# Kernel optimization log

Hardware: AMD Instinct MI355X
Metric: run time of the kernel (lower is better)

## Reference

```python
import math
import jax, jax.numpy as jnp
import numpy as np

B, LA, LB, H = 16, 1024, 1024, 512
NEG = -10000000.0


def setup_inputs() -> dict:
    key = jax.random.key(0)
    k1, k2, k3, k4 = jax.random.split(key, 4)
    a = jax.random.normal(k1, (B, LA, H), dtype=jnp.float32)
    b = jax.random.normal(k2, (B, LB, H), dtype=jnp.float32)
    mask_a = jax.random.randint(k3, (B, LA, 1), 0, 2, dtype=jnp.int32)
    mask_b = jax.random.randint(k4, (B, LB, 1), 0, 2, dtype=jnp.int32)
    temperature = jnp.asarray(1.0 / math.sqrt(H), dtype=jnp.float32)
    return {"a": a, "b": b, "mask_a": mask_a, "mask_b": mask_b, "temperature": temperature}


def reference(a, b, mask_a, mask_b, temperature):
    # attn[b,i,j] = <a_i, b_j> * temperature  -> [B, LA, LB]
    attn = jnp.einsum("bid,bjd->bij", a, b) * temperature
    # pairwise validity mask: outer product of per-token masks
    mask = jnp.einsum("bik,bjk->bij", mask_a.astype(jnp.float32), mask_b.astype(jnp.float32)) > 0
    attn = jnp.where(mask, attn, NEG)
    attn_a = jax.nn.softmax(attn, axis=1)  # softmax over a-tokens
    attn_b = jax.nn.softmax(attn, axis=2)  # softmax over b-tokens
    feature_b = jnp.einsum("bij,bid->bjd", attn_a, a)  # [B, LB, H]
    feature_a = jnp.einsum("bij,bjd->bid", attn_b, b)  # [B, LA, H]
    return (feature_a, feature_b)
```

## Files before the change

kernel.cpp:

```cpp
#include <hip/hip_runtime.h>
#include <hip/hip_bf16.h>

#define NB_ 16
#define LA_ 1024
#define LB_ 1024
#define H_  512

typedef __attribute__((ext_vector_type(8))) short short8;
typedef __attribute__((ext_vector_type(4))) float f32x4;

using bf16 = __hip_bfloat16;

__device__ __forceinline__ float bf2f(unsigned short u) {
    union { unsigned int i; float f; } c; c.i = ((unsigned)u) << 16; return c.f;
}
__device__ __forceinline__ unsigned short f2bf(float f) {
    bf16 h = __float2bfloat16(f);
    return *(unsigned short*)&h;
}

__device__ __forceinline__ void load_lds16(const void* g, void* l) {
    __builtin_amdgcn_global_load_lds(
        (const __attribute__((address_space(1))) void*)g,
        (__attribute__((address_space(3))) void*)l, 16, 0, 0);
}

template<int DB, int MODE>
__device__ __forceinline__ void gemm_tile256(
    const unsigned short* __restrict__ gA, const unsigned short* __restrict__ gB,
    int lda, int ldb, size_t ko,
    unsigned short* lds, char* lA, char* lB,
    const int* aoff, const int* boff, f32x4 acc[8][4])
{
    const char* bA = (const char*)lds + DB * 32768;
    const char* bB = (const char*)lds + 65536 + DB * 32768;
    const int nxt = (DB ^ 1) * 32768;
    short8 av[4][2];
#pragma unroll
    for (int p = 0; p < 4; ++p) {
        const int pm = p >> 1, pn = p & 1;
        if (pn == 0) {
#pragma unroll
            for (int f = 0; f < 4; f++)
#pragma unroll
                for (int kk = 0; kk < 2; kk++)
                    av[f][kk] = *(const short8*)(bA + (aoff[pm * 4 + f] ^ (kk << 6)));
        }
        short8 bv[2][2];
#pragma unroll
        for (int f = 0; f < 2; f++)
#pragma unroll
            for (int kk = 0; kk < 2; kk++)
                bv[f][kk] = *(const short8*)(bB + (boff[pn * 2 + f] ^ (kk << 6)));
        if (MODE == 0) {
            if (p == 0) {
                load_lds16(gB + ko,                       lB + nxt);
                load_lds16(gB + ko + (size_t)64 * ldb,    lB + nxt + 8192);
            } else if (p == 1) {
                load_lds16(gB + ko + (size_t)128 * ldb,   lB + nxt + 16384);
                load_lds16(gB + ko + (size_t)192 * ldb,   lB + nxt + 24576);
            } else if (p == 2) {
                load_lds16(gA + ko,                       lA + nxt);
                load_lds16(gA + ko + (size_t)128 * lda,   lA + nxt + 16384);
            } else {
                load_lds16(gA + ko + (size_t)64 * lda,    lA + nxt + 8192);
                load_lds16(gA + ko + (size_t)192 * lda,   lA + nxt + 24576);
            }
        }
        __builtin_amdgcn_s_barrier();
        __builtin_amdgcn_s_setprio(1);
#pragma unroll
        for (int kk = 0; kk < 2; kk++)
#pragma unroll
            for (int f = 0; f < 2; f++)
#pragma unroll
                for (int m = 0; m < 4; m++)
                    acc[pm * 4 + m][pn * 2 + f] =
                        __builtin_amdgcn_mfma_f32_16x16x32_bf16(
                            av[m][kk], bv[f][kk],
                            acc[pm * 4 + m][pn * 2 + f], 0, 0, 0);
        __builtin_amdgcn_s_setprio(0);
        if (p == 1) {
            if (MODE == 0) asm volatile("s_waitcnt vmcnt(4)" ::: "memory");
            else           asm volatile("s_waitcnt vmcnt(0)" ::: "memory");
        }
        if (p == 3 && MODE == 0) asm volatile("s_waitcnt vmcnt(2)" ::: "memory");
        if (p < 3 || MODE == 0) __builtin_amdgcn_s_barrier();
    }
}

__device__ __forceinline__ void gemm_core256(
    const unsigned short* __restrict__ A, const unsigned short* __restrict__ B,
    int lda, int ldb, int K,
    unsigned short* lds, f32x4 acc[8][4])
{
    const int t = threadIdx.x;
    const int w = t >> 6, lane = t & 63;
    const int wr = w >> 2, wc = w & 3;
    const int lm = lane & 15, q = lane >> 4;

    int aoff[8], boff[4];
#pragma unroll
    for (int f = 0; f < 8; f++) {
        const int ra = wr * 128 + f * 16 + lm;
        aoff[f] = ra * 128 + ((q ^ (ra & 7)) << 4);
    }
#pragma unroll
    for (int f = 0; f < 4; f++) {
        const int rb = wc * 64 + f * 16 + lm;
        boff[f] = rb * 128 + ((q ^ (rb & 7)) << 4);
    }

    const int rstep = w * 8 + (lane >> 3);
    const int sc = (lane & 7) ^ (lane >> 3);
    const unsigned short* gA = A + (size_t)rstep * lda + sc * 8;
    const unsigned short* gB = B + (size_t)rstep * ldb + sc * 8;
    char* lA = (char*)lds + w * 1024;
    char* lB = (char*)lds + 65536 + w * 1024;
    const int NT = K >> 6;

    load_lds16(gB,                       lB);
    load_lds16(gB + (size_t)64 * ldb,    lB + 8192);
    load_lds16(gB + (size_t)128 * ldb,   lB + 16384);
    load_lds16(gB + (size_t)192 * ldb,   lB + 24576);
    load_lds16(gA,                       lA);
    load_lds16(gA + (size_t)128 * lda,   lA + 16384);
    load_lds16(gA + (size_t)64 * lda,    lA + 8192);
    load_lds16(gA + (size_t)192 * lda,   lA + 24576);
    asm volatile("s_waitcnt vmcnt(2)" ::: "memory");
    __builtin_amdgcn_s_barrier();

    int kt = 0;
    for (; kt + 2 < NT; kt += 2) {
        gemm_tile256<0, 0>(gA, gB, lda, ldb, (size_t)(kt + 1) * 64,
                           lds, lA, lB, aoff, boff, acc);
        gemm_tile256<1, 0>(gA, gB, lda, ldb, (size_t)(kt + 2) * 64,
                           lds, lA, lB, aoff, boff, acc);
    }
    gemm_tile256<0, 0>(gA, gB, lda, ldb, (size_t)(NT - 1) * 64,
                       lds, lA, lB, aoff, boff, acc);
    gemm_tile256<1, 1>(gA, gB, lda, ldb, 0, lds, lA, lB, aoff, boff, acc);
    __syncthreads();
}

__global__ __launch_bounds__(512, 2) void k_gemm_attn(
    const unsigned short* __restrict__ a_bf, const unsigned short* __restrict__ b_bf,
    const int* __restrict__ mask_a, const int* __restrict__ mask_b,
    const float* __restrict__ temp_p,
    unsigned short* __restrict__ E, unsigned short* __restrict__ ET,
    float* __restrict__ l_row, float* __restrict__ l_col)
{
    __shared__ unsigned short lds[65536];

    const int g = blockIdx.x;
    const int batch = g & 15;
    const int qq = g >> 4;
    const int i0 = (qq >> 2) * 256, j0 = (qq & 3) * 256;

    const unsigned short* A = a_bf + (size_t)batch * LA_ * H_ + (size_t)i0 * H_;
    const unsigned short* B = b_bf + (size_t)batch * LB_ * H_ + (size_t)j0 * H_;
    f32x4 acc[8][4];
#pragma unroll
    for (int x = 0; x < 8; x++)
#pragma unroll
        for (int y = 0; y < 4; y++) acc[x][y] = 0;

    gemm_core256(A, B, H_, H_, H_, lds, acc);

    const float temp = temp_p[0];
    const int t = threadIdx.x, w = t >> 6, lane = t & 63;
    const int wr = w >> 2, wc = w & 3, lm = lane & 15, q = lane >> 4;
    const int* map = mask_a + batch * LA_;
    const int* mbp = mask_b + batch * LB_;
    unsigned short* Ep  = E  + (size_t)batch * LA_ * LB_;
    unsigned short* ETp = ET + (size_t)batch * LB_ * LA_;
    float* lrp = l_row + batch * LA_;
    float* lcp = l_col + batch * LB_;

    int mb4[4];
#pragma unroll
    for (int fn = 0; fn < 4; fn++) mb4[fn] = mbp[j0 + wc * 64 + fn * 16 + lm];

#pragma unroll
    for (int fm = 0; fm < 8; fm++) {
        const int ilb = wr * 128 + fm * 16 + q * 4;
        int ma[4];
#pragma unroll
        for (int r = 0; r < 4; r++) ma[r] = map[i0 + ilb + r];
#pragma unroll
        for (int fn = 0; fn < 4; fn++) {
            const int jl = wc * 64 + fn * 16 + lm;
            ushort4 pk;
            unsigned short* pp = (unsigned short*)&pk;
#pragma unroll
            for (int r = 0; r < 4; r++) {
                const float e = (ma[r] && mb4[fn]) ? __expf(acc[fm][fn][r] * temp) : 0.0f;
                acc[fm][fn][r] = e;
                pp[r] = f2bf(e);
                const int il = ilb + r;
                lds[il * 256 + ((((jl >> 3) ^ ((il >> 1) & 15)) << 3) | (jl & 7))] = pp[r];
            }
            *(ushort4*)(ETp + (size_t)(j0 + jl) * LA_ + i0 + ilb) = pk;
        }
    }

#pragma unroll
    for (int fm = 0; fm < 8; fm++)
#pragma unroll
        for (int r = 0; r < 4; r++) {
            float s = acc[fm][0][r] + acc[fm][1][r] + acc[fm][2][r] + acc[fm][3][r];
            s += __shfl_xor(s, 1, 16); s += __shfl_xor(s, 2, 16);
            s += __shfl_xor(s, 4, 16); s += __shfl_xor(s, 8, 16);
            if (lm == 0) atomicAdd(&lrp[i0 + wr * 128 + fm * 16 + q * 4 + r], s);
        }
#pragma unroll
    for (int fn = 0; fn < 4; fn++) {
        float s = 0.0f;
#pragma unroll
        for (int fm = 0; fm < 8; fm++)
#pragma unroll
            for (int r = 0; r < 4; r++) s += acc[fm][fn][r];
        s += __shfl_xor(s, 16, 64); s += __shfl_xor(s, 32, 64);
        if (lane < 16) atomicAdd(&lcp[j0 + wc * 64 + fn * 16 + lm], s);
    }

    __syncthreads();
#pragma unroll
    for (int rep = 0; rep < 16; rep++) {
        const int il = (t >> 5) + rep * 16;
        const int c = t & 31;
        const int phys = c ^ ((il >> 1) & 15);
        short8 v = *(const short8*)(lds + il * 256 + phys * 8);
        *(short8*)(Ep + (size_t)(i0 + il) * LB_ + j0 + c * 8) = v;
    }
}

__global__ __launch_bounds__(512, 2) void k_gemm_feat(
    const unsigned short* __restrict__ E, const unsigned short* __restrict__ ET,
    const unsigned short* __restrict__ aT, const unsigned short* __restrict__ bT,
    const int* __restrict__ mask_a, const int* __restrict__ mask_b,
    const int* __restrict__ nA, const int* __restrict__ nB,
    const float* __restrict__ l_row, const float* __restrict__ l_col,
    const float* __restrict__ mean_a, const float* __restrict__ mean_b,
    float* __restrict__ out)
{
    __shared__ unsigned short lds[65536];

    const int g = blockIdx.x;
    const int zc = g & 31;
    const int qq = g >> 5;
    const int n0 = (qq & 1) * 256, m0 = (qq >> 1) * 256;

    const int batch = zc & 15;
    const bool isA = zc < 16;
    const unsigned short* Amat = (isA ? E : ET) + (size_t)batch * 1024 * 1024;
    const unsigned short* Bm   = (isA ? bT : aT) + (size_t)batch * H_ * 1024;
    const int* mp   = (isA ? mask_a : mask_b) + batch * 1024;
    const int nn    = (isA ? nB : nA)[batch];
    const float* sp = (isA ? l_row : l_col) + batch * 1024;
    const float* mv = (isA ? mean_b : mean_a) + batch * H_;
    float* op = out + (isA ? (size_t)0 : (size_t)NB_ * LA_ * H_) + (size_t)batch * 1024 * H_;

    f32x4 acc[8][4];
#pragma unroll
    for (int x = 0; x < 8; x++)
#pragma unroll
        for (int y = 0; y < 4; y++) acc[x][y] = 0;

    gemm_core256(Amat + (size_t)m0 * 1024, Bm + (size_t)n0 * 1024,
                 1024, 1024, 1024, lds, acc);

    const int t = threadIdx.x, w = t >> 6, lane = t & 63;
    const int wr = w >> 2, wc = w & 3, lm = lane & 15, q = lane >> 4;

    float mval[4];
#pragma unroll
    for (int fn = 0; fn < 4; fn++) mval[fn] = mv[n0 + wc * 64 + fn * 16 + lm];

#pragma unroll
    for (int fm = 0; fm < 8; fm++) {
        const int ib = m0 + wr * 128 + fm * 16 + q * 4;
#pragma unroll
        for (int r = 0; r < 4; r++) {
            const int i = ib + r;
            const bool valid = (mp[i] != 0) && (nn > 0);
            const float inv = valid ? 1.0f / sp[i] : 0.0f;
#pragma unroll
            for (int fn = 0; fn < 4; fn++) {
                const int d = n0 + wc * 64 + fn * 16 + lm;
                op[(size_t)i * H_ + d] = valid ? acc[fm][fn][r] * inv : mval[fn];
            }
        }
    }
}

__global__ __launch_bounds__(256) void k_prep(
    const float* __restrict__ a, const float* __restrict__ b,
    unsigned short* __restrict__ aN, unsigned short* __restrict__ bN,
    unsigned short* __restrict__ aT, unsigned short* __restrict__ bT,
    float* __restrict__ mean_a, float* __restrict__ mean_b)
{
    __shared__ unsigned short lds[64][68];
    __shared__ float smean[64];
    const int z = blockIdx.z;
    const int batch = z & 15, sel = z >> 4;
    const float* src = sel ? b : a;
    unsigned short* np = (sel ? bN : aN) + (size_t)batch * 1024 * H_;
    unsigned short* tp = (sel ? bT : aT) + (size_t)batch * H_ * 1024;
    float* mdst = (sel ? mean_b : mean_a) + batch * H_;
    const float* sp = src + (size_t)batch * 1024 * H_;

    const int d0 = blockIdx.x * 64, i0 = blockIdx.y * 64;
    const int t = threadIdx.x;
    if (t < 64) smean[t] = 0.0f;
    const int c4 = (t & 15) * 4;
#pragma unroll
    for (int it = 0; it < 4; it++) {
        const int r = (t >> 4) + it * 16;
        float4 v = *(const float4*)(sp + (size_t)(i0 + r) * H_ + d0 + c4);
        ushort4 u = make_ushort4(f2bf(v.x), f2bf(v.y), f2bf(v.z), f2bf(v.w));
        *(ushort4*)(np + (size_t)(i0 + r) * H_ + d0 + c4) = u;
        *(ushort4*)&lds[r][c4] = u;
    }
    __syncthreads();
#pragma unroll
    for (int it = 0; it < 4; it++) {
        const int dd = (t >> 4) + it * 16;
        const int i4 = (t & 15) * 4;
        ushort4 u = make_ushort4(lds[i4][dd], lds[i4 + 1][dd], lds[i4 + 2][dd], lds[i4 + 3][dd]);
        *(ushort4*)(tp + (size_t)(d0 + dd) * 1024 + i0 + i4) = u;
        atomicAdd(&smean[dd], bf2f(u.x) + bf2f(u.y) + bf2f(u.z) + bf2f(u.w));
    }
    __syncthreads();
    if (t < 64) atomicAdd(&mdst[d0 + t], smean[t] * (1.0f / 1024.0f));
}

__global__ __launch_bounds__(256) void k_init(
    float* __restrict__ accum_zero,
    const int* __restrict__ mask_a, const int* __restrict__ mask_b,
    int* __restrict__ nA, int* __restrict__ nB)
{
    const int g = blockIdx.x, t = threadIdx.x;
    if (g < 48) {
        *(float4*)(accum_zero + (size_t)(g * 256 + t) * 4) = make_float4(0, 0, 0, 0);
        return;
    }
    const int sel = g - 48;
    const int batch = sel & 15, which = sel >> 4;
    const int* m = (which ? mask_b : mask_a) + batch * 1024;
    int s = m[t] + m[t + 256] + m[t + 512] + m[t + 768];
    __shared__ int red[256];
    red[t] = s;
    __syncthreads();
    for (int off = 128; off; off >>= 1) {
        if (t < off) red[t] += red[t + off];
        __syncthreads();
    }
    if (t == 0) (which ? nB : nA)[batch] = red[0];
}

extern "C" void kernel_launch(void* const* d_in, const int* in_sizes, int n_in,
                              void* d_out, int out_size, void* d_ws, size_t ws_size,
                              hipStream_t stream)
{
    const float* a      = (const float*)d_in[0];
    const float* b      = (const float*)d_in[1];
    const int*   mask_a = (const int*)d_in[2];
    const int*   mask_b = (const int*)d_in[3];
    const float* temp   = (const float*)d_in[4];
    float* out = (float*)d_out;

    char* ws = (char*)d_ws;
    size_t off = 0;
    unsigned short* E    = (unsigned short*)(ws + off); off += (size_t)NB_ * LA_ * LB_ * 2;
    unsigned short* ET   = (unsigned short*)(ws + off); off += (size_t)NB_ * LB_ * LA_ * 2;
    unsigned short* a_bf = (unsigned short*)(ws + off); off += (size_t)NB_ * LA_ * H_ * 2;
    unsigned short* b_bf = (unsigned short*)(ws + off); off += (size_t)NB_ * LB_ * H_ * 2;
    unsigned short* aT   = (unsigned short*)(ws + off); off += (size_t)NB_ * H_ * LA_ * 2;
    unsigned short* bT   = (unsigned short*)(ws + off); off += (size_t)NB_ * H_ * LB_ * 2;
    float* l_row  = (float*)(ws + off); off += (size_t)NB_ * LA_ * 4;
    float* l_col  = (float*)(ws + off); off += (size_t)NB_ * LB_ * 4;
    float* mean_a = (float*)(ws + off); off += (size_t)NB_ * H_ * 4;
    float* mean_b = (float*)(ws + off); off += (size_t)NB_ * H_ * 4;
    int*   nA     = (int*)(ws + off); off += 64;
    int*   nB     = (int*)(ws + off); off += 64;

    k_init<<<dim3(80), 256, 0, stream>>>(l_row, mask_a, mask_b, nA, nB);

    k_prep<<<dim3(H_ / 64, 1024 / 64, 32), 256, 0, stream>>>(
        a, b, a_bf, b_bf, aT, bT, mean_a, mean_b);

    k_gemm_attn<<<dim3(256), 512, 0, stream>>>(
        a_bf, b_bf, mask_a, mask_b, temp, E, ET, l_row, l_col);

    k_gemm_feat<<<dim3(256), 512, 0, stream>>>(
        E, ET, aT, bT, mask_a, mask_b, nA, nB, l_row, l_col, mean_a, mean_b, out);
}
```

Measured before the change: 215.3 us.

## Merge init into prep with per-strip column sums; add drain-style GEMM schedule

```diff
diff --git a/kernel.cpp b/kernel.cpp
--- a/kernel.cpp
+++ b/kernel.cpp
@@ -26,7 +26,7 @@
 }
 
 template<int DB, int MODE>
-__device__ __forceinline__ void gemm_tile256(
+__device__ __forceinline__ void gemm_tile_cnt(
     const unsigned short* __restrict__ gA, const unsigned short* __restrict__ gB,
     int lda, int ldb, size_t ko,
     unsigned short* lds, char* lA, char* lB,
@@ -89,6 +89,59 @@
     }
 }
 
+template<int DB, int MODE>
+__device__ __forceinline__ void gemm_tile_drn(
+    const unsigned short* __restrict__ gA, const unsigned short* __restrict__ gB,
+    int lda, int ldb, size_t ko,
+    unsigned short* lds, char* lA, char* lB,
+    const int* aoff, const int* boff, f32x4 acc[8][4])
+{
+    const char* bA = (const char*)lds + DB * 32768;
+    const char* bB = (const char*)lds + 65536 + DB * 32768;
+    const int nxt = (DB ^ 1) * 32768;
+    if (MODE == 0) {
+#pragma unroll
+        for (int s = 0; s < 4; s++) {
+            load_lds16(gA + ko + (size_t)(s * 64) * lda, lA + nxt + s * 8192);
+            load_lds16(gB + ko + (size_t)(s * 64) * ldb, lB + nxt + s * 8192);
+        }
+    }
+    short8 av[4][2];
+#pragma unroll
+    for (int p = 0; p < 4; ++p) {
+        const int pm = p >> 1, pn = p & 1;
+        if (pn == 0) {
+#pragma unroll
+            for (int f = 0; f < 4; f++)
+#pragma unroll
+                for (int kk = 0; kk < 2; kk++)
+                    av[f][kk] = *(const short8*)(bA + (aoff[pm * 4 + f] ^ (kk << 6)));
+        }
+        short8 bv[2][2];
+#pragma unroll
+        for (int f = 0; f < 2; f++)
+#pragma unroll
+            for (int kk = 0; kk < 2; kk++)
+                bv[f][kk] = *(const short8*)(bB + (boff[pn * 2 + f] ^ (kk << 6)));
+        __builtin_amdgcn_s_barrier();
+        __builtin_amdgcn_s_setprio(1);
+#pragma unroll
+        for (int kk = 0; kk < 2; kk++)
+#pragma unroll
+            for (int f = 0; f < 2; f++)
+#pragma unroll
+                for (int m = 0; m < 4; m++)
+                    acc[pm * 4 + m][pn * 2 + f] =
+                        __builtin_amdgcn_mfma_f32_16x16x32_bf16(
+                            av[m][kk], bv[f][kk],
+                            acc[pm * 4 + m][pn * 2 + f], 0, 0, 0);
+        __builtin_amdgcn_s_setprio(0);
+        if (p < 3) __builtin_amdgcn_s_barrier();
+    }
+    __syncthreads();
+}
+
+template<int SCHED>
 __device__ __forceinline__ void gemm_core256(
     const unsigned short* __restrict__ A, const unsigned short* __restrict__ B,
     int lda, int ldb, int K,
@@ -119,27 +172,45 @@
     char* lB = (char*)lds + 65536 + w * 1024;
     const int NT = K >> 6;
 
-    load_lds16(gB,                       lB);
-    load_lds16(gB + (size_t)64 * ldb,    lB + 8192);
-    load_lds16(gB + (size_t)128 * ldb,   lB + 16384);
-    load_lds16(gB + (size_t)192 * ldb,   lB + 24576);
-    load_lds16(gA,                       lA);
-    load_lds16(gA + (size_t)128 * lda,   lA + 16384);
-    load_lds16(gA + (size_t)64 * lda,    lA + 8192);
-    load_lds16(gA + (size_t)192 * lda,   lA + 24576);
-    asm volatile("s_waitcnt vmcnt(2)" ::: "memory");
-    __builtin_amdgcn_s_barrier();
-
-    int kt = 0;
-    for (; kt + 2 < NT; kt += 2) {
-        gemm_tile256<0, 0>(gA, gB, lda, ldb, (size_t)(kt + 1) * 64,
-                           lds, lA, lB, aoff, boff, acc);
-        gemm_tile256<1, 0>(gA, gB, lda, ldb, (size_t)(kt + 2) * 64,
-                           lds, lA, lB, aoff, boff, acc);
-    }
-    gemm_tile256<0, 0>(gA, gB, lda, ldb, (size_t)(NT - 1) * 64,
-                       lds, lA, lB, aoff, boff, acc);
-    gemm_tile256<1, 1>(gA, gB, lda, ldb, 0, lds, lA, lB, aoff, boff, acc);
+    if (SCHED == 0) {
+        load_lds16(gB,                       lB);
+        load_lds16(gB + (size_t)64 * ldb,    lB + 8192);
+        load_lds16(gB + (size_t)128 * ldb,   lB + 16384);
+        load_lds16(gB + (size_t)192 * ldb,   lB + 24576);
+        load_lds16(gA,                       lA);
+        load_lds16(gA + (size_t)128 * lda,   lA + 16384);
+        load_lds16(gA + (size_t)64 * lda,    lA + 8192);
+        load_lds16(gA + (size_t)192 * lda,   lA + 24576);
+        asm volatile("s_waitcnt vmcnt(2)" ::: "memory");
+        __builtin_amdgcn_s_barrier();
+        int kt = 0;
+        for (; kt + 2 < NT; kt += 2) {
+            gemm_tile_cnt<0, 0>(gA, gB, lda, ldb, (size_t)(kt + 1) * 64,
+                                lds, lA, lB, aoff, boff, acc);
+            gemm_tile_cnt<1, 0>(gA, gB, lda, ldb, (size_t)(kt + 2) * 64,
+                                lds, lA, lB, aoff, boff, acc);
+        }
+        gemm_tile_cnt<0, 0>(gA, gB, lda, ldb, (size_t)(NT - 1) * 64,
+                            lds, lA, lB, aoff, boff, acc);
+        gemm_tile_cnt<1, 1>(gA, gB, lda, ldb, 0, lds, lA, lB, aoff, boff, acc);
+    } else {
+#pragma unroll
+        for (int s = 0; s < 4; s++) {
+            load_lds16(gA + (size_t)(s * 64) * lda, lA + s * 8192);
+            load_lds16(gB + (size_t)(s * 64) * ldb, lB + s * 8192);
+        }
+        __syncthreads();
+        int kt = 0;
+        for (; kt + 2 < NT; kt += 2) {
+            gemm_tile_drn<0, 0>(gA, gB, lda, ldb, (size_t)(kt + 1) * 64,
+                                lds, lA, lB, aoff, boff, acc);
+            gemm_tile_drn<1, 0>(gA, gB, lda, ldb, (size_t)(kt + 2) * 64,
+                                lds, lA, lB, aoff, boff, acc);
+        }
+        gemm_tile_drn<0, 0>(gA, gB, lda, ldb, (size_t)(NT - 1) * 64,
+                            lds, lA, lB, aoff, boff, acc);
+        gemm_tile_drn<1, 1>(gA, gB, lda, ldb, 0, lds, lA, lB, aoff, boff, acc);
+    }
     __syncthreads();
 }
 
@@ -165,7 +236,7 @@
 #pragma unroll
         for (int y = 0; y < 4; y++) acc[x][y] = 0;
 
-    gemm_core256(A, B, H_, H_, H_, lds, acc);
+    gemm_core256<1>(A, B, H_, H_, H_, lds, acc);
 
     const float temp = temp_p[0];
     const int t = threadIdx.x, w = t >> 6, lane = t & 63;
@@ -267,8 +338,8 @@
 #pragma unroll
         for (int y = 0; y < 4; y++) acc[x][y] = 0;
 
-    gemm_core256(Amat + (size_t)m0 * 1024, Bm + (size_t)n0 * 1024,
-                 1024, 1024, 1024, lds, acc);
+    gemm_core256<0>(Amat + (size_t)m0 * 1024, Bm + (size_t)n0 * 1024,
+                    1024, 1024, 1024, lds, acc);
 
     const int t = threadIdx.x, w = t >> 6, lane = t & 63;
     const int wr = w >> 2, wc = w & 3, lm = lane & 15, q = lane >> 4;
@@ -298,65 +369,72 @@
     const float* __restrict__ a, const float* __restrict__ b,
     unsigned short* __restrict__ aN, unsigned short* __restrict__ bN,
     unsigned short* __restrict__ aT, unsigned short* __restrict__ bT,
-    float* __restrict__ mean_a, float* __restrict__ mean_b)
-{
-    __shared__ unsigned short lds[64][68];
-    __shared__ float smean[64];
-    const int z = blockIdx.z;
-    const int batch = z & 15, sel = z >> 4;
-    const float* src = sel ? b : a;
+    float* __restrict__ mean_a, float* __restrict__ mean_b,
+    const int* __restrict__ mask_a, const int* __restrict__ mask_b,
+    int* __restrict__ nA, int* __restrict__ nB,
+    float* __restrict__ zero_base)
+{
+    const int g = blockIdx.x, t = threadIdx.x;
+    if (g >= 256) {
+        const int s = g - 256;
+        *(float4*)(zero_base + ((size_t)s * 256 + t) * 4) = make_float4(0, 0, 0, 0);
+        const int batch = s & 15, which = s >> 4;
+        const int* m = (which ? mask_b : mask_a) + batch * 1024;
+        int cnt = m[t] + m[t + 256] + m[t + 512] + m[t + 768];
+        __shared__ int red[256];
+        red[t] = cnt;
+        __syncthreads();
+        for (int off = 128; off; off >>= 1) {
+            if (t < off) red[t] += red[t + off];
+            __syncthreads();
+        }
+        if (t == 0) (which ? nB : nA)[batch] = red[0];
+        return;
+    }
+    const int dstrip = g & 7, batch = (g >> 3) & 15, sel = g >> 7;
+    const float* src = (sel ? b : a) + (size_t)batch * 1024 * H_;
     unsigned short* np = (sel ? bN : aN) + (size_t)batch * 1024 * H_;
     unsigned short* tp = (sel ? bT : aT) + (size_t)batch * H_ * 1024;
     float* mdst = (sel ? mean_b : mean_a) + batch * H_;
-    const float* sp = src + (size_t)batch * 1024 * H_;
-
-    const int d0 = blockIdx.x * 64, i0 = blockIdx.y * 64;
-    const int t = threadIdx.x;
-    if (t < 64) smean[t] = 0.0f;
+    const int d0 = dstrip * 64;
+
+    __shared__ unsigned short lds[64][68];
+    __shared__ float cs[4][64];
     const int c4 = (t & 15) * 4;
-#pragma unroll
-    for (int it = 0; it < 4; it++) {
-        const int r = (t >> 4) + it * 16;
-        float4 v = *(const float4*)(sp + (size_t)(i0 + r) * H_ + d0 + c4);
-        ushort4 u = make_ushort4(f2bf(v.x), f2bf(v.y), f2bf(v.z), f2bf(v.w));
-        *(ushort4*)(np + (size_t)(i0 + r) * H_ + d0 + c4) = u;
-        *(ushort4*)&lds[r][c4] = u;
+    float colsum[4] = {0.f, 0.f, 0.f, 0.f};
+    for (int i0 = 0; i0 < 1024; i0 += 64) {
+#pragma unroll
+        for (int it = 0; it < 4; it++) {
+            const int r = (t >> 4) + it * 16;
+            float4 v = *(const float4*)(src + (size_t)(i0 + r) * H_ + d0 + c4);
+            colsum[0] += v.x; colsum[1] += v.y; colsum[2] += v.z; colsum[3] += v.w;
+            ushort4 u = make_ushort4(f2bf(v.x), f2bf(v.y), f2bf(v.z), f2bf(v.w));
+            *(ushort4*)(np + (size_t)(i0 + r) * H_ + d0 + c4) = u;
+            *(ushort4*)&lds[r][c4] = u;
+        }
+        __syncthreads();
+#pragma unroll
+        for (int it = 0; it < 4; it++) {
+            const int dd = (t >> 4) + it * 16;
+            const int i4 = (t & 15) * 4;
+            ushort4 u = make_ushort4(lds[i4][dd], lds[i4 + 1][dd],
+                                     lds[i4 + 2][dd], lds[i4 + 3][dd]);
+            *(ushort4*)(tp + (size_t)(d0 + dd) * 1024 + i0 + i4) = u;
+        }
+        __syncthreads();
+    }
+#pragma unroll
+    for (int j = 0; j < 4; j++) {
+        colsum[j] += __shfl_xor(colsum[j], 16, 64);
+        colsum[j] += __shfl_xor(colsum[j], 32, 64);
+    }
+    const int w = t >> 6, lane = t & 63;
+    if (lane < 16) {
+#pragma unroll
+        for (int j = 0; j < 4; j++) cs[w][c4 + j] = colsum[j];
     }
     __syncthreads();
-#pragma unroll
-    for (int it = 0; it < 4; it++) {
-        const int dd = (t >> 4) + it * 16;
-        const int i4 = (t & 15) * 4;
-        ushort4 u = make_ushort4(lds[i4][dd], lds[i4 + 1][dd], lds[i4 + 2][dd], lds[i4 + 3][dd]);
-        *(ushort4*)(tp + (size_t)(d0 + dd) * 1024 + i0 + i4) = u;
-        atomicAdd(&smean[dd], bf2f(u.x) + bf2f(u.y) + bf2f(u.z) + bf2f(u.w));
-    }
-    __syncthreads();
-    if (t < 64) atomicAdd(&mdst[d0 + t], smean[t] * (1.0f / 1024.0f));
-}
-
-__global__ __launch_bounds__(256) void k_init(
-    float* __restrict__ accum_zero,
-    const int* __restrict__ mask_a, const int* __restrict__ mask_b,
-    int* __restrict__ nA, int* __restrict__ nB)
-{
-    const int g = blockIdx.x, t = threadIdx.x;
-    if (g < 48) {
-        *(float4*)(accum_zero + (size_t)(g * 256 + t) * 4) = make_float4(0, 0, 0, 0);
-        return;
-    }
-    const int sel = g - 48;
-    const int batch = sel & 15, which = sel >> 4;
-    const int* m = (which ? mask_b : mask_a) + batch * 1024;
-    int s = m[t] + m[t + 256] + m[t + 512] + m[t + 768];
-    __shared__ int red[256];
-    red[t] = s;
-    __syncthreads();
-    for (int off = 128; off; off >>= 1) {
-        if (t < off) red[t] += red[t + off];
-        __syncthreads();
-    }
-    if (t == 0) (which ? nB : nA)[batch] = red[0];
+    if (t < 64) mdst[d0 + t] = (cs[0][t] + cs[1][t] + cs[2][t] + cs[3][t]) * (1.0f / 1024.0f);
 }
 
 extern "C" void kernel_launch(void* const* d_in, const int* in_sizes, int n_in,
@@ -385,10 +463,9 @@
     int*   nA     = (int*)(ws + off); off += 64;
     int*   nB     = (int*)(ws + off); off += 64;
 
-    k_init<<<dim3(80), 256, 0, stream>>>(l_row, mask_a, mask_b, nA, nB);
-
-    k_prep<<<dim3(H_ / 64, 1024 / 64, 32), 256, 0, stream>>>(
-        a, b, a_bf, b_bf, aT, bT, mean_a, mean_b);
+    k_prep<<<dim3(288), 256, 0, stream>>>(
+        a, b, a_bf, b_bf, aT, bT, mean_a, mean_b,
+        mask_a, mask_b, nA, nB, l_row);
 
     k_gemm_attn<<<dim3(256), 512, 0, stream>>>(
         a_bf, b_bf, mask_a, mask_b, temp, E, ET, l_row, l_col);
```

Result: faster. 203.1 us (-5.7%).
